# Optimization experiments

Measured on AMD Instinct MI355X. Metric: run time of the kernel, lower is better.

Reference implementation:

```python
import jax, jax.numpy as jnp
import numpy as np

B, S, D, H = 4, 2048, 2048, 16
DH = D // H


def setup_inputs() -> dict:
    key = jax.random.key(0)
    ks = jax.random.split(key, 11)
    p = 0.02  # keep pre-softmax logits in a sane range
    return {
        "x": jax.random.normal(ks[0], (B, S, D), jnp.float32),
        "Wq": jax.random.normal(ks[1], (D, D), jnp.float32) * p,
        "bq": jax.random.normal(ks[2], (D,), jnp.float32) * p,
        "Wk": jax.random.normal(ks[3], (D, D), jnp.float32) * p,
        "bk": jax.random.normal(ks[4], (D,), jnp.float32) * p,
        "Wv": jax.random.normal(ks[5], (D, D), jnp.float32) * p,
        "bv": jax.random.normal(ks[6], (D,), jnp.float32) * p,
        "Wo": jax.random.normal(ks[7], (D, D), jnp.float32) * p,
        "bo": jax.random.normal(ks[8], (D,), jnp.float32) * p,
        "spiral_weight": jax.random.normal(ks[9], (H,), jnp.float32),
        "helix_rotation": jax.random.normal(ks[10], (D,), jnp.float32),
    }


def reference(x, Wq, bq, Wk, bk, Wv, bv, Wo, bo, spiral_weight, helix_rotation):
    b, s, d = x.shape
    h, dh = H, d // H
    # projections (torch Linear: x @ W.T + b), split into heads
    q = (x @ Wq.T + bq).reshape(b, s, h, dh)
    k = (x @ Wk.T + bk).reshape(b, s, h, dh)
    v = (x @ Wv.T + bv).reshape(b, s, h, dh)
    # cos/sin helix gating, applied per (head, head_dim) channel
    rot = helix_rotation.reshape(h, dh)
    q = q * jnp.cos(rot)
    k = k * jnp.sin(rot)
    # per-head scaled scores: [b,h,s,s]
    scores = jnp.einsum("bshd,bthd->bhst", q, k) / np.sqrt(dh).astype(np.float32)
    scores = scores * spiral_weight[None, :, None, None]
    attn = jax.nn.softmax(scores, axis=-1)
    out = jnp.einsum("bhst,bthd->bshd", attn, v).reshape(b, s, d)
    return out @ Wo.T + bo
```

## Files before the change

kernel.cpp:

```cpp
#include <hip/hip_runtime.h>
#include <math.h>

#define B_ 4
#define S_ 2048
#define D_ 2048
#define H_ 16
#define DH_ 128

typedef unsigned short u16;
typedef unsigned int u32;
typedef u16 u16x8 __attribute__((ext_vector_type(8)));
typedef __bf16 bf16x8 __attribute__((ext_vector_type(8)));
typedef float f32x4 __attribute__((ext_vector_type(4)));

__device__ inline u16 f2bf(float f) {
    unsigned int u = __builtin_bit_cast(unsigned int, f);
    unsigned int lsb = (u >> 16) & 1u;
    u += 0x7fffu + lsb;
    return (u16)(u >> 16);
}

__device__ inline f32x4 mfma16(u16x8 a, u16x8 b, f32x4 c) {
    return __builtin_amdgcn_mfma_f32_16x16x32_bf16(
        __builtin_bit_cast(bf16x8, a), __builtin_bit_cast(bf16x8, b), c, 0, 0, 0);
}

__device__ inline void gl2lds16(const u16* g, u16* l) {
    __builtin_amdgcn_global_load_lds(
        (const __attribute__((address_space(1))) void*)g,
        (__attribute__((address_space(3))) void*)l, 16, 0, 0);
}

__global__ __launch_bounds__(256) void cvt_f32_bf16(const float* __restrict__ src,
                                                    u16* __restrict__ dst, int n8) {
    int i = blockIdx.x * 256 + threadIdx.x;
    if (i >= n8) return;
    const float4* s = (const float4*)src + (size_t)i * 2;
    float4 a = s[0], b = s[1];
    u16x8 o;
    o[0] = f2bf(a.x); o[1] = f2bf(a.y); o[2] = f2bf(a.z); o[3] = f2bf(a.w);
    o[4] = f2bf(b.x); o[5] = f2bf(b.y); o[6] = f2bf(b.z); o[7] = f2bf(b.w);
    *((u16x8*)dst + i) = o;
}

template <int GATE, int TRANSV, typename OutT>
__global__ __launch_bounds__(256) void gemm_bt(const u16* __restrict__ A,
                                               const u16* __restrict__ Bw,
                                               const float* __restrict__ bias,
                                               const float* __restrict__ helix,
                                               OutT* __restrict__ C,
                                               int M, int N, int K) {
    __shared__ __align__(16) u16 As[128 * 64];
    __shared__ __align__(16) u16 Bs[128 * 64];

    const int tid = threadIdx.x;
    const int lane = tid & 63, w = tid >> 6;
    const int lr = lane & 15, quad = lane >> 4;
    const int wm = w & 1, wn = w >> 1;
    const int tm = blockIdx.y, tn = blockIdx.x;

    const u16* Ab = A + (size_t)(tm * 128) * K;
    const u16* Bb = Bw + (size_t)(tn * 128) * K;

    const u16* gA[4];
    const u16* gB[4];
    u16* lA[4];
    u16* lB[4];
#pragma unroll
    for (int q = 0; q < 4; ++q) {
        int seg = w * 4 + q;
        int row = seg * 8 + (lane >> 3);
        int gcol = ((lane & 7) ^ (row & 7)) * 8;
        gA[q] = Ab + (size_t)row * K + gcol;
        gB[q] = Bb + (size_t)row * K + gcol;
        lA[q] = As + seg * 512;
        lB[q] = Bs + seg * 512;
    }

    f32x4 zero = {0.f, 0.f, 0.f, 0.f};
    f32x4 acc[4][4];
#pragma unroll
    for (int im = 0; im < 4; ++im)
#pragma unroll
        for (int jn = 0; jn < 4; ++jn) acc[im][jn] = zero;

    const int rA = wm * 64 + lr;
    const int rB = wn * 64 + lr;
    const int sw = lr & 7;

    for (int kt = 0; kt < K; kt += 64) {
        __syncthreads();
#pragma unroll
        for (int q = 0; q < 4; ++q) gl2lds16(gA[q] + kt, lA[q]);
#pragma unroll
        for (int q = 0; q < 4; ++q) gl2lds16(gB[q] + kt, lB[q]);
        __syncthreads();

#pragma unroll
        for (int s = 0; s < 2; ++s) {
            const int kc = ((s * 4 + quad) ^ sw) * 8;
            u16x8 af[4], bf[4];
#pragma unroll
            for (int im = 0; im < 4; ++im)
                af[im] = *(const u16x8*)&As[(rA + im * 16) * 64 + kc];
#pragma unroll
            for (int jn = 0; jn < 4; ++jn)
                bf[jn] = *(const u16x8*)&Bs[(rB + jn * 16) * 64 + kc];
#pragma unroll
            for (int im = 0; im < 4; ++im)
#pragma unroll
                for (int jn = 0; jn < 4; ++jn)
                    acc[im][jn] = mfma16(af[im], bf[jn], acc[im][jn]);
        }
    }

    if constexpr (TRANSV) {
        __shared__ __align__(16) u16 Ts[128 * 72];
        const int grow = tm * 128;
        const int bb = grow / S_;
        const int t0g = grow % S_;
#pragma unroll
        for (int hb = 0; hb < 2; ++hb) {
            __syncthreads();
            if (wm == hb) {
#pragma unroll
                for (int jn = 0; jn < 4; ++jn) {
                    float bs = bias[tn * 128 + wn * 64 + jn * 16 + lr];
#pragma unroll
                    for (int im = 0; im < 4; ++im)
#pragma unroll
                        for (int r = 0; r < 4; ++r)
                            Ts[(wn * 64 + jn * 16 + lr) * 72 + im * 16 + quad * 4 + r] =
                                f2bf(acc[im][jn][r] + bs);
                }
            }
            __syncthreads();
#pragma unroll
            for (int p = 0; p < 4; ++p) {
                int idx = p * 256 + tid;
                int dh_l = idx & 127, tb8 = idx >> 7;
                u16x8 o = *(const u16x8*)&Ts[dh_l * 72 + tb8 * 8];
                int gd = tn * 128 + dh_l;
                int hh = gd >> 7, dhm = gd & 127;
                u16* dst = (u16*)C + (((size_t)bb * H_ + hh) * DH_ + dhm) * S_ + t0g +
                           hb * 64 + tb8 * 8;
                *(u16x8*)dst = o;
            }
        }
    } else {
#pragma unroll
        for (int jn = 0; jn < 4; ++jn) {
            int col = tn * 128 + wn * 64 + jn * 16 + lr;
            float bs = bias[col];
            float g = 1.0f;
            if (GATE == 1) g = cosf(helix[col]);
            if (GATE == 2) g = sinf(helix[col]);
#pragma unroll
            for (int im = 0; im < 4; ++im)
#pragma unroll
                for (int r = 0; r < 4; ++r) {
                    int row = tm * 128 + wm * 64 + im * 16 + quad * 4 + r;
                    float val = (acc[im][jn][r] + bs) * g;
                    if constexpr (sizeof(OutT) == 2)
                        ((u16*)C)[(size_t)row * N + col] = f2bf(val);
                    else
                        ((float*)C)[(size_t)row * N + col] = val;
                }
        }
    }
}

__global__ __launch_bounds__(256, 2) void helix_attn(const u16* __restrict__ Q,
                                                     const u16* __restrict__ Kq,
                                                     const u16* __restrict__ Vt,
                                                     const float* __restrict__ spiral,
                                                     u16* __restrict__ O) {
    __shared__ __align__(16) u16 Ks[64 * 136];
    __shared__ __align__(16) u16 Vs[128 * 72];
    __shared__ __align__(16) u16 Ps[128 * 80];

    const int tid = threadIdx.x;
    const int lane = tid & 63, w = tid >> 6;
    const int lr = lane & 15, quad = lane >> 4;

    const int bx = blockIdx.x;
    const int qt = bx & 15;
    const int h = (bx >> 4) & 15;
    const int b = bx >> 8;

    const size_t headoff = (size_t)b * S_ * D_ + (size_t)h * DH_;
    const u16* qp = Q + headoff;
    const u16* kp = Kq + headoff;
    const u16* vtp = Vt + ((size_t)b * H_ + h) * (size_t)DH_ * S_;

    const float scale2 = spiral[h] * 0.08838834764831845f * 1.4426950408889634f;

    u16x8 qf[2][4];
#pragma unroll
    for (int mb = 0; mb < 2; ++mb)
#pragma unroll
        for (int c = 0; c < 4; ++c) {
            u16x8 raw = *(const u16x8*)(qp + (size_t)(qt * 128 + mb * 64 + w * 16 + lr) * D_ +
                                        c * 32 + quad * 8);
#pragma unroll
            for (int j = 0; j < 8; ++j) {
                float f = __builtin_bit_cast(float, (u32)raw[j] << 16) * scale2;
                qf[mb][c][j] = f2bf(f);
            }
        }

    f32x4 zero = {0.f, 0.f, 0.f, 0.f};
    f32x4 Oacc[2][8];
#pragma unroll
    for (int mb = 0; mb < 2; ++mb)
#pragma unroll
        for (int n = 0; n < 8; ++n) Oacc[mb][n] = zero;
    float rs[2][4] = {{0.f, 0.f, 0.f, 0.f}, {0.f, 0.f, 0.f, 0.f}};

    for (int tt = 0; tt < 32; ++tt) {
        const int t0 = tt * 64;
        __syncthreads();
#pragma unroll
        for (int p = 0; p < 4; ++p) {
            int lin = p * 256 + tid;
            int trow = lin >> 4;
            int ch = (lin & 15) * 8;
            *(u16x8*)&Ks[trow * 136 + ch] =
                *(const u16x8*)(kp + (size_t)(t0 + trow) * D_ + ch);
            int drow = lin >> 3;
            int tch = (lin & 7) * 8;
            *(u16x8*)&Vs[drow * 72 + tch] =
                *(const u16x8*)(vtp + (size_t)drow * S_ + t0 + tch);
        }
        __syncthreads();

        f32x4 Sacc[2][4] = {{zero, zero, zero, zero}, {zero, zero, zero, zero}};
#pragma unroll
        for (int c = 0; c < 4; ++c) {
#pragma unroll
            for (int j = 0; j < 4; ++j) {
                u16x8 kf = *(const u16x8*)&Ks[(j * 16 + lr) * 136 + c * 32 + quad * 8];
                Sacc[0][j] = mfma16(qf[0][c], kf, Sacc[0][j]);
                Sacc[1][j] = mfma16(qf[1][c], kf, Sacc[1][j]);
            }
        }

#pragma unroll
        for (int mb = 0; mb < 2; ++mb)
#pragma unroll
            for (int j = 0; j < 4; ++j)
#pragma unroll
                for (int r = 0; r < 4; ++r) {
                    float p = exp2f(Sacc[mb][j][r]);
                    u32 u = __builtin_bit_cast(u32, p);
                    rs[mb][r] += __builtin_bit_cast(float, u & 0xffff0000u);
                    Ps[(mb * 64 + w * 16 + quad * 4 + r) * 80 + j * 16 + lr] = (u16)(u >> 16);
                }

#pragma unroll
        for (int ks = 0; ks < 2; ++ks) {
            u16x8 pf0 = *(const u16x8*)&Ps[(w * 16 + lr) * 80 + ks * 32 + quad * 8];
            u16x8 pf1 = *(const u16x8*)&Ps[(64 + w * 16 + lr) * 80 + ks * 32 + quad * 8];
#pragma unroll
            for (int n = 0; n < 8; ++n) {
                u16x8 vf = *(const u16x8*)&Vs[(n * 16 + lr) * 72 + ks * 32 + quad * 8];
                Oacc[0][n] = mfma16(pf0, vf, Oacc[0][n]);
                Oacc[1][n] = mfma16(pf1, vf, Oacc[1][n]);
            }
        }
    }

#pragma unroll
    for (int mb = 0; mb < 2; ++mb)
#pragma unroll
        for (int r = 0; r < 4; ++r) {
            float s = rs[mb][r];
#pragma unroll
            for (int off = 1; off < 16; off <<= 1) s += __shfl_xor(s, off, 64);
            float inv = 1.0f / s;
            int row = qt * 128 + mb * 64 + w * 16 + quad * 4 + r;
            u16* op = O + headoff + (size_t)row * D_;
#pragma unroll
            for (int n = 0; n < 8; ++n) op[n * 16 + lr] = f2bf(Oacc[mb][n][r] * inv);
        }
}

extern "C" void kernel_launch(void* const* d_in, const int* in_sizes, int n_in,
                              void* d_out, int out_size, void* d_ws, size_t ws_size,
                              hipStream_t stream) {
    const float* x = (const float*)d_in[0];
    const float* Wq = (const float*)d_in[1];
    const float* bq = (const float*)d_in[2];
    const float* Wk = (const float*)d_in[3];
    const float* bk = (const float*)d_in[4];
    const float* Wv = (const float*)d_in[5];
    const float* bv = (const float*)d_in[6];
    const float* Wo = (const float*)d_in[7];
    const float* bo = (const float*)d_in[8];
    const float* spiral = (const float*)d_in[9];
    const float* helix = (const float*)d_in[10];
    float* out = (float*)d_out;

    char* ws = (char*)d_ws;
    u16* xbf = (u16*)(ws);
    u16* wqb = (u16*)(ws + 33554432);
    u16* wkb = (u16*)(ws + 33554432 + 8388608);
    u16* wvb = (u16*)(ws + 33554432 + 16777216);
    u16* wob = (u16*)(ws + 33554432 + 25165824);
    u16* qb = (u16*)(ws + 67108864);
    u16* kb = (u16*)(ws + 67108864 + 33554432);
    u16* vtb = (u16*)(ws + 67108864 + 67108864);
    u16* attnb = xbf;

    const int ND = D_ * D_;
    const int NX = B_ * S_ * D_;

    cvt_f32_bf16<<<NX / 8 / 256, 256, 0, stream>>>(x, xbf, NX / 8);
    cvt_f32_bf16<<<ND / 8 / 256, 256, 0, stream>>>(Wq, wqb, ND / 8);
    cvt_f32_bf16<<<ND / 8 / 256, 256, 0, stream>>>(Wk, wkb, ND / 8);
    cvt_f32_bf16<<<ND / 8 / 256, 256, 0, stream>>>(Wv, wvb, ND / 8);
    cvt_f32_bf16<<<ND / 8 / 256, 256, 0, stream>>>(Wo, wob, ND / 8);

    dim3 gg(D_ / 128, (B_ * S_) / 128);
    gemm_bt<1, 0, u16><<<gg, 256, 0, stream>>>(xbf, wqb, bq, helix, qb, B_ * S_, D_, D_);
    gemm_bt<2, 0, u16><<<gg, 256, 0, stream>>>(xbf, wkb, bk, helix, kb, B_ * S_, D_, D_);
    gemm_bt<0, 1, u16><<<gg, 256, 0, stream>>>(xbf, wvb, bv, nullptr, vtb, B_ * S_, D_, D_);

    helix_attn<<<B_ * H_ * (S_ / 128), 256, 0, stream>>>(qb, kb, vtb, spiral, attnb);

    gemm_bt<0, 0, float><<<gg, 256, 0, stream>>>(attnb, wob, bo, nullptr, out, B_ * S_, D_, D_);
}
```

Baseline: 704.2 us.

## Swizzle attention LDS tiles, use direct global-to-LDS loads, fuse conversion kernels

The attention kernel drops padded LDS tiles in favour of XOR-swizzled layouts and loads K/V tiles with global_load_lds direct-to-LDS copies. QK^T now computes the transposed score tile, so each lane holds a row of P and writes it as packed u32x2 stores; row sums become per-lane scalars reduced with fewer shuffles. LDS use shrinks and launch bounds rise to 3 blocks per CU to raise occupancy, and exp2 uses the hardware builtin. The five f32-to-bf16 conversion launches are merged into one kernel, at the risk of register pressure under the tighter launch bound.

```diff
diff --git a/kernel.cpp b/kernel.cpp
--- a/kernel.cpp
+++ b/kernel.cpp
@@ -12,6 +12,13 @@
 typedef u16 u16x8 __attribute__((ext_vector_type(8)));
 typedef __bf16 bf16x8 __attribute__((ext_vector_type(8)));
 typedef float f32x4 __attribute__((ext_vector_type(4)));
+typedef u32 u32x2 __attribute__((ext_vector_type(2)));
+
+#if __has_builtin(__builtin_amdgcn_exp2f)
+#define EXP2(x) __builtin_amdgcn_exp2f(x)
+#else
+#define EXP2(x) exp2f(x)
+#endif
 
 __device__ inline u16 f2bf(float f) {
     unsigned int u = __builtin_bit_cast(unsigned int, f);
@@ -31,16 +38,29 @@
         (__attribute__((address_space(3))) void*)l, 16, 0, 0);
 }
 
-__global__ __launch_bounds__(256) void cvt_f32_bf16(const float* __restrict__ src,
-                                                    u16* __restrict__ dst, int n8) {
+__global__ __launch_bounds__(256) void cvt_all(const float* __restrict__ x,
+                                               const float* __restrict__ Wq,
+                                               const float* __restrict__ Wk,
+                                               const float* __restrict__ Wv,
+                                               const float* __restrict__ Wo,
+                                               u16* __restrict__ xbf, u16* __restrict__ wqb,
+                                               u16* __restrict__ wkb, u16* __restrict__ wvb,
+                                               u16* __restrict__ wob) {
     int i = blockIdx.x * 256 + threadIdx.x;
-    if (i >= n8) return;
-    const float4* s = (const float4*)src + (size_t)i * 2;
+    const float* src;
+    u16* dst;
+    int off;
+    if (i < 2097152) { src = x;  dst = xbf; off = i; }
+    else if (i < 2621440) { src = Wq; dst = wqb; off = i - 2097152; }
+    else if (i < 3145728) { src = Wk; dst = wkb; off = i - 2621440; }
+    else if (i < 3670016) { src = Wv; dst = wvb; off = i - 3145728; }
+    else { src = Wo; dst = wob; off = i - 3670016; }
+    const float4* s = (const float4*)src + (size_t)off * 2;
     float4 a = s[0], b = s[1];
     u16x8 o;
     o[0] = f2bf(a.x); o[1] = f2bf(a.y); o[2] = f2bf(a.z); o[3] = f2bf(a.w);
     o[4] = f2bf(b.x); o[5] = f2bf(b.y); o[6] = f2bf(b.z); o[7] = f2bf(b.w);
-    *((u16x8*)dst + i) = o;
+    *((u16x8*)dst + off) = o;
 }
 
 template <int GATE, int TRANSV, typename OutT>
@@ -170,18 +190,19 @@
     }
 }
 
-__global__ __launch_bounds__(256, 2) void helix_attn(const u16* __restrict__ Q,
+__global__ __launch_bounds__(256, 3) void helix_attn(const u16* __restrict__ Q,
                                                      const u16* __restrict__ Kq,
                                                      const u16* __restrict__ Vt,
                                                      const float* __restrict__ spiral,
                                                      u16* __restrict__ O) {
-    __shared__ __align__(16) u16 Ks[64 * 136];
-    __shared__ __align__(16) u16 Vs[128 * 72];
-    __shared__ __align__(16) u16 Ps[128 * 80];
+    __shared__ __align__(16) u16 Ks[64 * 128];
+    __shared__ __align__(16) u16 Vs[128 * 64];
+    __shared__ __align__(16) u16 Ps[128 * 64];
 
     const int tid = threadIdx.x;
     const int lane = tid & 63, w = tid >> 6;
     const int lr = lane & 15, quad = lane >> 4;
+    const int sw = lr & 7;
 
     const int bx = blockIdx.x;
     const int qt = bx & 15;
@@ -195,6 +216,21 @@
 
     const float scale2 = spiral[h] * 0.08838834764831845f * 1.4426950408889634f;
 
+    const u16* gK[4];
+    const u16* gV[4];
+    u16* lK[4];
+    u16* lV[4];
+#pragma unroll
+    for (int q = 0; q < 4; ++q) {
+        int seg = w * 4 + q;
+        int rowK = seg * 4 + (lane >> 4);
+        gK[q] = kp + (size_t)rowK * D_ + (((lane & 15) ^ (rowK & 7)) * 8);
+        lK[q] = Ks + seg * 512;
+        int rowV = seg * 8 + (lane >> 3);
+        gV[q] = vtp + (size_t)rowV * S_ + (((lane & 7) ^ (rowV & 7)) * 8);
+        lV[q] = Vs + seg * 512;
+    }
+
     u16x8 qf[2][4];
 #pragma unroll
     for (int mb = 0; mb < 2; ++mb)
@@ -215,55 +251,56 @@
     for (int mb = 0; mb < 2; ++mb)
 #pragma unroll
         for (int n = 0; n < 8; ++n) Oacc[mb][n] = zero;
-    float rs[2][4] = {{0.f, 0.f, 0.f, 0.f}, {0.f, 0.f, 0.f, 0.f}};
+    float rs[2] = {0.f, 0.f};
 
     for (int tt = 0; tt < 32; ++tt) {
-        const int t0 = tt * 64;
         __syncthreads();
 #pragma unroll
-        for (int p = 0; p < 4; ++p) {
-            int lin = p * 256 + tid;
-            int trow = lin >> 4;
-            int ch = (lin & 15) * 8;
-            *(u16x8*)&Ks[trow * 136 + ch] =
-                *(const u16x8*)(kp + (size_t)(t0 + trow) * D_ + ch);
-            int drow = lin >> 3;
-            int tch = (lin & 7) * 8;
-            *(u16x8*)&Vs[drow * 72 + tch] =
-                *(const u16x8*)(vtp + (size_t)drow * S_ + t0 + tch);
-        }
+        for (int q = 0; q < 4; ++q) gl2lds16(gK[q] + (size_t)tt * 64 * D_, lK[q]);
+#pragma unroll
+        for (int q = 0; q < 4; ++q) gl2lds16(gV[q] + tt * 64, lV[q]);
         __syncthreads();
 
         f32x4 Sacc[2][4] = {{zero, zero, zero, zero}, {zero, zero, zero, zero}};
 #pragma unroll
-        for (int c = 0; c < 4; ++c) {
-#pragma unroll
-            for (int j = 0; j < 4; ++j) {
-                u16x8 kf = *(const u16x8*)&Ks[(j * 16 + lr) * 136 + c * 32 + quad * 8];
-                Sacc[0][j] = mfma16(qf[0][c], kf, Sacc[0][j]);
-                Sacc[1][j] = mfma16(qf[1][c], kf, Sacc[1][j]);
-            }
-        }
-
-#pragma unroll
-        for (int mb = 0; mb < 2; ++mb)
-#pragma unroll
-            for (int j = 0; j < 4; ++j)
-#pragma unroll
-                for (int r = 0; r < 4; ++r) {
-                    float p = exp2f(Sacc[mb][j][r]);
-                    u32 u = __builtin_bit_cast(u32, p);
-                    rs[mb][r] += __builtin_bit_cast(float, u & 0xffff0000u);
-                    Ps[(mb * 64 + w * 16 + quad * 4 + r) * 80 + j * 16 + lr] = (u16)(u >> 16);
-                }
+        for (int c = 0; c < 4; ++c)
+#pragma unroll
+            for (int tj = 0; tj < 4; ++tj) {
+                u16x8 kf = *(const u16x8*)&Ks[(tj * 16 + lr) * 128 + (((4 * c + quad) ^ sw) * 8)];
+                Sacc[0][tj] = mfma16(kf, qf[0][c], Sacc[0][tj]);
+                Sacc[1][tj] = mfma16(kf, qf[1][c], Sacc[1][tj]);
+            }
+
+        u32* Pw = (u32*)Ps;
+#pragma unroll
+        for (int mb = 0; mb < 2; ++mb) {
+            const int rowdw = (mb * 64 + w * 16 + lr) * 32;
+#pragma unroll
+            for (int tj = 0; tj < 4; ++tj) {
+                u32 u0 = __builtin_bit_cast(u32, EXP2(Sacc[mb][tj][0]));
+                u32 u1 = __builtin_bit_cast(u32, EXP2(Sacc[mb][tj][1]));
+                u32 u2 = __builtin_bit_cast(u32, EXP2(Sacc[mb][tj][2]));
+                u32 u3 = __builtin_bit_cast(u32, EXP2(Sacc[mb][tj][3]));
+                rs[mb] += __builtin_bit_cast(float, u0 & 0xffff0000u) +
+                          __builtin_bit_cast(float, u1 & 0xffff0000u) +
+                          __builtin_bit_cast(float, u2 & 0xffff0000u) +
+                          __builtin_bit_cast(float, u3 & 0xffff0000u);
+                u32x2 pk;
+                pk[0] = (u0 >> 16) | (u1 & 0xffff0000u);
+                pk[1] = (u2 >> 16) | (u3 & 0xffff0000u);
+                int dw = rowdw + (((2 * tj + (quad >> 1)) ^ sw) * 4) + 2 * (quad & 1);
+                *(u32x2*)&Pw[dw] = pk;
+            }
+        }
 
 #pragma unroll
         for (int ks = 0; ks < 2; ++ks) {
-            u16x8 pf0 = *(const u16x8*)&Ps[(w * 16 + lr) * 80 + ks * 32 + quad * 8];
-            u16x8 pf1 = *(const u16x8*)&Ps[(64 + w * 16 + lr) * 80 + ks * 32 + quad * 8];
+            const int gk = ((4 * ks + quad) ^ sw) * 8;
+            u16x8 pf0 = *(const u16x8*)&Ps[(w * 16 + lr) * 64 + gk];
+            u16x8 pf1 = *(const u16x8*)&Ps[(64 + w * 16 + lr) * 64 + gk];
 #pragma unroll
             for (int n = 0; n < 8; ++n) {
-                u16x8 vf = *(const u16x8*)&Vs[(n * 16 + lr) * 72 + ks * 32 + quad * 8];
+                u16x8 vf = *(const u16x8*)&Vs[(n * 16 + lr) * 64 + gk];
                 Oacc[0][n] = mfma16(pf0, vf, Oacc[0][n]);
                 Oacc[1][n] = mfma16(pf1, vf, Oacc[1][n]);
             }
@@ -271,18 +308,20 @@
     }
 
 #pragma unroll
-    for (int mb = 0; mb < 2; ++mb)
+    for (int mb = 0; mb < 2; ++mb) {
+        float s = rs[mb];
+        s += __shfl_xor(s, 16, 64);
+        s += __shfl_xor(s, 32, 64);
 #pragma unroll
         for (int r = 0; r < 4; ++r) {
-            float s = rs[mb][r];
-#pragma unroll
-            for (int off = 1; off < 16; off <<= 1) s += __shfl_xor(s, off, 64);
-            float inv = 1.0f / s;
+            float sv = __shfl(s, quad * 4 + r, 64);
+            float inv = 1.0f / sv;
             int row = qt * 128 + mb * 64 + w * 16 + quad * 4 + r;
             u16* op = O + headoff + (size_t)row * D_;
 #pragma unroll
             for (int n = 0; n < 8; ++n) op[n * 16 + lr] = f2bf(Oacc[mb][n][r] * inv);
         }
+    }
 }
 
 extern "C" void kernel_launch(void* const* d_in, const int* in_sizes, int n_in,
@@ -312,14 +351,7 @@
     u16* vtb = (u16*)(ws + 67108864 + 67108864);
     u16* attnb = xbf;
 
-    const int ND = D_ * D_;
-    const int NX = B_ * S_ * D_;
-
-    cvt_f32_bf16<<<NX / 8 / 256, 256, 0, stream>>>(x, xbf, NX / 8);
-    cvt_f32_bf16<<<ND / 8 / 256, 256, 0, stream>>>(Wq, wqb, ND / 8);
-    cvt_f32_bf16<<<ND / 8 / 256, 256, 0, stream>>>(Wk, wkb, ND / 8);
-    cvt_f32_bf16<<<ND / 8 / 256, 256, 0, stream>>>(Wv, wvb, ND / 8);
-    cvt_f32_bf16<<<ND / 8 / 256, 256, 0, stream>>>(Wo, wob, ND / 8);
+    cvt_all<<<4194304 / 256, 256, 0, stream>>>(x, Wq, Wk, Wv, Wo, xbf, wqb, wkb, wvb, wob);
 
     dim3 gg(D_ / 128, (B_ * S_) / 128);
     gemm_bt<1, 0, u16><<<gg, 256, 0, stream>>>(xbf, wqb, bq, helix, qb, B_ * S_, D_, D_);
```

New measurement: 726.9 us. 1.03x slower.
